# Performance work log

Measured on AMD Instinct MI355X. Metric: run time of the kernel, lower is better.

Reference implementation:

```python
import jax, jax.numpy as jnp
import numpy as np

R_MAX = 1.0
BASIS_MASK = 0xFF        # low 8 bits -> basis index (basis_size=256)
R_BITS_MASK = 0xFFFF     # next 16 bits -> quantized radius
R_DENOM = 65535.0
INT8_DENOM = 127.0


def setup_inputs() -> dict:
    key = jax.random.key(0)
    k_x, k_c, k_b, k_r, k_s, k_bias = jax.random.split(key, 6)
    B, S, D_in, D_out, BASIS = 4, 2048, 4096, 4096, 256
    x = jax.random.normal(k_x, (B, S, D_in), dtype=jnp.float32)
    codes = jax.random.randint(k_c, (D_out,), 0, 16777216, dtype=jnp.int32)
    basis_table = jax.random.normal(k_b, (BASIS, D_in), dtype=jnp.float32)
    residual_q = jax.random.randint(k_r, (D_out, D_in), 0, 256, dtype=jnp.int32)
    residual_scales = jax.random.uniform(k_s, (D_out,), dtype=jnp.float32) * 0.05
    bias = jax.random.normal(k_bias, (D_out,), dtype=jnp.float32)
    return {"x": x, "codes": codes, "basis_table": basis_table,
            "residual_q": residual_q, "residual_scales": residual_scales,
            "bias": bias}


def decode_weight(codes, basis_table, residual_q, residual_scales):
    # Bitfield decode: low 8 bits = basis index, next 16 bits = quantized radius in [0, r_max].
    idx = codes & BASIS_MASK                                   # [O]
    r = ((codes >> 8) & R_BITS_MASK).astype(jnp.float32) / R_DENOM * R_MAX  # [O]
    base = r[:, None] * basis_table[idx]                       # [O, I]
    resid = (residual_q.astype(jnp.float32) - 128.0) / INT8_DENOM  # dequant int8 residual
    return base + residual_scales[:, None] * resid             # [O, I]


def reference(x, codes, basis_table, residual_q, residual_scales, bias):
    W = decode_weight(codes, basis_table, residual_q, residual_scales)  # [O, I]
    # y = x @ W^T + bias  (fused dequant-matmul in the original CUDA kernel)
    return jnp.einsum("bsi,oi->bso", x, W) + bias
```

## Files before the change

### kernel.cpp

```cpp
#include <hip/hip_runtime.h>


typedef __bf16 bf16x8 __attribute__((ext_vector_type(8)));
typedef float f32x4 __attribute__((ext_vector_type(4)));
typedef int i32x4 __attribute__((ext_vector_type(4)));
typedef unsigned short u16x8 __attribute__((ext_vector_type(8)));

__device__ __forceinline__ unsigned short f2bf(float f) {
    union { float f; unsigned int u; } c; c.f = f;
    unsigned int u = c.u;
    u += 0x7fffu + ((u >> 16) & 1u);
    return (unsigned short)(u >> 16);
}
__device__ __forceinline__ float bf2f(unsigned short h) {
    union { unsigned int u; float f; } c; c.u = ((unsigned int)h) << 16;
    return c.f;
}

__device__ __forceinline__ void load_lds16(const void* g, void* l) {
    __builtin_amdgcn_global_load_lds(
        (__attribute__((address_space(1))) void*)(void*)g,
        (__attribute__((address_space(3))) void*)l,
        16, 0, 0);
}

__device__ __forceinline__ int swz_decode(int p, int row_bytes) {
    const int g = p >> 3, t = p & 7, v = t ^ (g & 7);
    const int row = g * 2 + (v >> 2), chunk = v & 3;
    return row * row_bytes + chunk * 16;
}

__global__ void cvt_bf16_kernel(const float4* __restrict__ in4,
                                ushort4* __restrict__ out4, int n4) {
    int i = blockIdx.x * blockDim.x + threadIdx.x;
    const int stride = gridDim.x * blockDim.x;
    for (; i < n4; i += stride) {
        float4 v = in4[i];
        ushort4 o;
        o.x = f2bf(v.x); o.y = f2bf(v.y); o.z = f2bf(v.z); o.w = f2bf(v.w);
        out4[i] = o;
    }
}

__global__ void quant_x_kernel(const float* __restrict__ x,
                               signed char* __restrict__ xq,
                               float* __restrict__ arow, int K) {
    const int m = blockIdx.x;
    const float* row = x + (size_t)m * K;
    const int base = threadIdx.x * 16;
    float4 v[4];
#pragma unroll
    for (int j = 0; j < 4; ++j) v[j] = *(const float4*)(row + base + j * 4);

    float lmax = 0.f;
#pragma unroll
    for (int j = 0; j < 4; ++j) {
        lmax = fmaxf(lmax, fabsf(v[j].x));
        lmax = fmaxf(lmax, fabsf(v[j].y));
        lmax = fmaxf(lmax, fabsf(v[j].z));
        lmax = fmaxf(lmax, fabsf(v[j].w));
    }
#pragma unroll
    for (int off = 32; off; off >>= 1)
        lmax = fmaxf(lmax, __shfl_xor(lmax, off));
    __shared__ float smax[4];
    if ((threadIdx.x & 63) == 0) smax[threadIdx.x >> 6] = lmax;
    __syncthreads();
    const float mx = fmaxf(fmaxf(smax[0], smax[1]), fmaxf(smax[2], smax[3]));
    const float inv = mx > 0.f ? 127.0f / mx : 0.0f;
    if (threadIdx.x == 0) arow[m] = mx * (1.0f / 127.0f);

    union { signed char c[16]; i32x4 w; } pk;
#pragma unroll
    for (int j = 0; j < 4; ++j) {
        pk.c[j * 4 + 0] = (signed char)(int)rintf(v[j].x * inv);
        pk.c[j * 4 + 1] = (signed char)(int)rintf(v[j].y * inv);
        pk.c[j * 4 + 2] = (signed char)(int)rintf(v[j].z * inv);
        pk.c[j * 4 + 3] = (signed char)(int)rintf(v[j].w * inv);
    }
    *(i32x4*)(xq + (size_t)m * K + base) = pk.w;
}

__global__ void pack_q_kernel(const int4* __restrict__ q4,
                              unsigned int* __restrict__ out, int n4) {
    const int i = blockIdx.x * blockDim.x + threadIdx.x;
    if (i >= n4) return;
    int4 a = q4[i];
    unsigned int w = ((unsigned)(a.x - 128) & 0xFFu)
                   | (((unsigned)(a.y - 128) & 0xFFu) << 8)
                   | (((unsigned)(a.z - 128) & 0xFFu) << 16)
                   | (((unsigned)(a.w - 128) & 0xFFu) << 24);
    out[i] = w;
}

__global__ void p_gemm_kernel(const unsigned short* __restrict__ Xb,
                              const unsigned short* __restrict__ Bb,
                              unsigned short* __restrict__ Pbf,
                              int M, int K) {
    __shared__ __align__(16) unsigned short As[64 * 32];
    __shared__ __align__(16) unsigned short Bs[64 * 32];

    const int tid  = threadIdx.x;
    const int lane = tid & 63;
    const int wv   = tid >> 6;
    const int m0 = blockIdx.y * 64;
    const int n0 = blockIdx.x * 64;
    const int lr = lane & 15;
    const int kg = lane >> 4;
    const int swz = (lr >> 1) & 7;

    f32x4 acc[4];
#pragma unroll
    for (int ni = 0; ni < 4; ++ni) acc[ni] = (f32x4){0.f, 0.f, 0.f, 0.f};

    const int goff = swz_decode(tid, 64);
    const unsigned short* Agp = Xb + (size_t)m0 * K + (goff >> 6) * K + ((goff & 63) >> 1);
    const unsigned short* Bgp = Bb + (size_t)n0 * K + (goff >> 6) * K + ((goff & 63) >> 1);
    unsigned short* Al = As + tid * 8;
    unsigned short* Bl = Bs + tid * 8;

    const int cidx = (((lr & 1) << 2) | kg) ^ swz;

    for (int k0 = 0; k0 < K; k0 += 32) {
        load_lds16(Agp + k0, Al);
        load_lds16(Bgp + k0, Bl);
        __syncthreads();

        const int arow2 = wv * 8 + (lr >> 1);
        bf16x8 af = __builtin_bit_cast(bf16x8,
            *(const u16x8*)(As + arow2 * 64 + cidx * 8));
#pragma unroll
        for (int ni = 0; ni < 4; ++ni) {
            const int brow2 = ni * 8 + (lr >> 1);
            bf16x8 bfr = __builtin_bit_cast(bf16x8,
                *(const u16x8*)(Bs + brow2 * 64 + cidx * 8));
            acc[ni] = __builtin_amdgcn_mfma_f32_16x16x32_bf16(af, bfr, acc[ni], 0, 0, 0);
        }
        __syncthreads();
    }

#pragma unroll
    for (int ni = 0; ni < 4; ++ni) {
        const int n = n0 + ni * 16 + lr;
        const int mbase = m0 + wv * 16 + kg * 4;
#pragma unroll
        for (int rg = 0; rg < 4; ++rg)
            Pbf[(size_t)(mbase + rg) * 256 + n] = f2bf(acc[ni][rg]);
    }
}

__global__ void gemm_i8_kernel(const signed char* __restrict__ Xq,
                               const signed char* __restrict__ Qb,
                               const float* __restrict__ arow,
                               const int* __restrict__ codes,
                               const float* __restrict__ scales,
                               const float* __restrict__ bias,
                               const unsigned short* __restrict__ Pbf,
                               float* __restrict__ out,
                               int M, int N, int K) {
    __shared__ __align__(16) signed char As[128 * 64];
    __shared__ __align__(16) signed char Bs[128 * 64];
    __shared__ unsigned short Pst[64 * 256];

    const int tid  = threadIdx.x;
    const int lane = tid & 63;
    const int wv   = tid >> 6;
    const int wrow = wv >> 1;
    const int wcol = wv & 1;
    const int m0 = blockIdx.y * 128;
    const int n0 = blockIdx.x * 128;
    const int lr = lane & 15;
    const int kg = lane >> 4;
    const int swz = (lr >> 1) & 7;
    const int cidx = (((lr & 1) << 2) | kg) ^ swz;

    int   cc[4];
    float rr[4], so[4], bv[4];
#pragma unroll
    for (int ni = 0; ni < 4; ++ni) {
        const int n = n0 + wcol * 64 + ni * 16 + lr;
        const int code = codes[n];
        cc[ni] = code & 0xFF;
        rr[ni] = (float)((code >> 8) & 0xFFFF) * (1.0f / 65535.0f);
        so[ni] = scales[n] * (1.0f / 127.0f);
        bv[ni] = bias[n];
    }
#pragma unroll
    for (int ni = 0; ni < 4; ++ni)
#pragma unroll
        for (int mi = 0; mi < 4; ++mi) {
            const int mb = m0 + wrow * 64 + mi * 16 + kg * 4;
#pragma unroll
            for (int rg = 0; rg < 4; ++rg) {
                unsigned short pv = Pbf[(size_t)(mb + rg) * 256 + cc[ni]];
                Pst[(ni * 16 + mi * 4 + rg) * 256 + tid] = pv;
            }
        }

    i32x4 acc[4][4];
#pragma unroll
    for (int mi = 0; mi < 4; ++mi)
#pragma unroll
        for (int ni = 0; ni < 4; ++ni)
            acc[mi][ni] = (i32x4){0, 0, 0, 0};

    const int p0 = tid, p1 = tid + 256;
    const int ga0 = swz_decode(p0, 64);
    const int ga1 = swz_decode(p1, 64);
    const signed char* Ag0 = Xq + (size_t)m0 * K + (ga0 >> 6) * K + (ga0 & 63);
    const signed char* Ag1 = Xq + (size_t)m0 * K + (ga1 >> 6) * K + (ga1 & 63);
    const signed char* Bg0 = Qb + (size_t)n0 * K + (ga0 >> 6) * K + (ga0 & 63);
    const signed char* Bg1 = Qb + (size_t)n0 * K + (ga1 >> 6) * K + (ga1 & 63);
    signed char* Al0 = As + p0 * 16;
    signed char* Al1 = As + p1 * 16;
    signed char* Bl0 = Bs + p0 * 16;
    signed char* Bl1 = Bs + p1 * 16;

    for (int k0 = 0; k0 < K; k0 += 64) {
        load_lds16(Ag0 + k0, Al0);
        load_lds16(Ag1 + k0, Al1);
        load_lds16(Bg0 + k0, Bl0);
        load_lds16(Bg1 + k0, Bl1);
        __syncthreads();

        i32x4 af[4], bfr[4];
#pragma unroll
        for (int mi = 0; mi < 4; ++mi) {
            const int r2 = wrow * 32 + mi * 8 + (lr >> 1);
            af[mi] = *(const i32x4*)(As + r2 * 128 + cidx * 16);
        }
#pragma unroll
        for (int ni = 0; ni < 4; ++ni) {
            const int r2 = wcol * 32 + ni * 8 + (lr >> 1);
            bfr[ni] = *(const i32x4*)(Bs + r2 * 128 + cidx * 16);
        }
#pragma unroll
        for (int mi = 0; mi < 4; ++mi)
#pragma unroll
            for (int ni = 0; ni < 4; ++ni)
                acc[mi][ni] = __builtin_amdgcn_mfma_i32_16x16x64_i8(
                    af[mi], bfr[ni], acc[mi][ni], 0, 0, 0);
        __syncthreads();
    }

    float av[4][4];
#pragma unroll
    for (int mi = 0; mi < 4; ++mi)
#pragma unroll
        for (int rg = 0; rg < 4; ++rg)
            av[mi][rg] = arow[m0 + wrow * 64 + mi * 16 + kg * 4 + rg];

#pragma unroll
    for (int ni = 0; ni < 4; ++ni) {
        const int n = n0 + wcol * 64 + ni * 16 + lr;
#pragma unroll
        for (int mi = 0; mi < 4; ++mi) {
            const int mbase = m0 + wrow * 64 + mi * 16 + kg * 4;
#pragma unroll
            for (int rg = 0; rg < 4; ++rg) {
                const float pf = bf2f(Pst[(ni * 16 + mi * 4 + rg) * 256 + tid]);
                const float y = av[mi][rg] * so[ni] * (float)acc[mi][ni][rg]
                              + rr[ni] * pf + bv[ni];
                __builtin_nontemporal_store(y, &out[(size_t)(mbase + rg) * N + n]);
            }
        }
    }
}

extern "C" void kernel_launch(void* const* d_in, const int* in_sizes, int n_in,
                              void* d_out, int out_size, void* d_ws, size_t ws_size,
                              hipStream_t stream) {
    const float* x        = (const float*)d_in[0];
    const int*   codes    = (const int*)d_in[1];
    const float* basis    = (const float*)d_in[2];
    const int*   q        = (const int*)d_in[3];
    const float* scales   = (const float*)d_in[4];
    const float* bias     = (const float*)d_in[5];
    float* out = (float*)d_out;

    const int BASIS = 256;
    const int K = in_sizes[2] / BASIS;
    const int N = in_sizes[1];
    const int M = in_sizes[0] / K;

    char* ws = (char*)d_ws;
    unsigned short* Xb = (unsigned short*)ws;
    signed char*    Xq = (signed char*)ws;
    size_t off = (size_t)M * K * 2;
    signed char* Qb = (signed char*)(ws + off);
    off += (size_t)N * K;
    unsigned short* Pbf = (unsigned short*)(ws + off);
    off += (size_t)M * 256 * 2;
    float* Arow = (float*)(ws + off);
    off += (size_t)M * sizeof(float);
    unsigned short* Bb = (unsigned short*)(ws + off);

    cvt_bf16_kernel<<<4096, 256, 0, stream>>>((const float4*)x, (ushort4*)Xb,
                                              M * K / 4);
    cvt_bf16_kernel<<<1024, 256, 0, stream>>>((const float4*)basis, (ushort4*)Bb,
                                              BASIS * K / 4);
    p_gemm_kernel<<<dim3(BASIS / 64, M / 64), 256, 0, stream>>>(Xb, Bb, Pbf, M, K);
    pack_q_kernel<<<(N * K / 4 + 255) / 256, 256, 0, stream>>>(
        (const int4*)q, (unsigned int*)Qb, N * K / 4);
    quant_x_kernel<<<M, 256, 0, stream>>>(x, Xq, Arow, K);
    gemm_i8_kernel<<<dim3(N / 128, M / 128), 256, 0, stream>>>(
        Xq, Qb, Arow, codes, scales, bias, Pbf, out, M, N, K);
}
```

Measured before the change: 535.2 us.

## Fuse x bf16 conversion into basis GEMM and enlarge int8 GEMM tile

The separate fp32-to-bf16 conversion pass over x is removed. The basis projection GEMM now loads fp32 x directly into LDS and converts it while building fragments, with each block covering all 256 basis columns for 32 rows. The int8 GEMM tile grows to 128x256 with launch bounds set for two blocks per CU and a swapped grid order. The LDS staging of gathered P values is dropped in favour of direct global loads in the epilogue. These changes cut memory traffic and launches, but they raise register pressure and turn the P gather into uncoalesced global reads.

```diff
diff --git a/kernel.cpp b/kernel.cpp
--- a/kernel.cpp
+++ b/kernel.cpp
@@ -93,151 +93,163 @@
     out[i] = w;
 }
 
-__global__ void p_gemm_kernel(const unsigned short* __restrict__ Xb,
-                              const unsigned short* __restrict__ Bb,
-                              unsigned short* __restrict__ Pbf,
-                              int M, int K) {
-    __shared__ __align__(16) unsigned short As[64 * 32];
-    __shared__ __align__(16) unsigned short Bs[64 * 32];
+__global__ __launch_bounds__(256) void
+p_gemm_kernel(const float* __restrict__ x,
+              const unsigned short* __restrict__ Bb,
+              unsigned short* __restrict__ Pbf,
+              int M, int K) {
+    __shared__ __align__(16) float As[32 * 64];
+    __shared__ __align__(16) unsigned short Bs[256 * 64];
 
     const int tid  = threadIdx.x;
     const int lane = tid & 63;
     const int wv   = tid >> 6;
-    const int m0 = blockIdx.y * 64;
-    const int n0 = blockIdx.x * 64;
+    const int m0 = blockIdx.x * 32;
     const int lr = lane & 15;
     const int kg = lane >> 4;
-    const int swz = (lr >> 1) & 7;
-
-    f32x4 acc[4];
-#pragma unroll
-    for (int ni = 0; ni < 4; ++ni) acc[ni] = (f32x4){0.f, 0.f, 0.f, 0.f};
-
-    const int goff = swz_decode(tid, 64);
-    const unsigned short* Agp = Xb + (size_t)m0 * K + (goff >> 6) * K + ((goff & 63) >> 1);
-    const unsigned short* Bgp = Bb + (size_t)n0 * K + (goff >> 6) * K + ((goff & 63) >> 1);
-    unsigned short* Al = As + tid * 8;
-    unsigned short* Bl = Bs + tid * 8;
-
-    const int cidx = (((lr & 1) << 2) | kg) ^ swz;
-
-    for (int k0 = 0; k0 < K; k0 += 32) {
-        load_lds16(Agp + k0, Al);
-        load_lds16(Bgp + k0, Bl);
+
+    f32x4 acc[2][4];
+#pragma unroll
+    for (int mi = 0; mi < 2; ++mi)
+#pragma unroll
+        for (int ni = 0; ni < 4; ++ni)
+            acc[mi][ni] = (f32x4){0.f, 0.f, 0.f, 0.f};
+
+    int aRow[2], aSrc[2];
+#pragma unroll
+    for (int j = 0; j < 2; ++j) {
+        const int p = tid + 256 * j;
+        aRow[j] = p >> 4;
+        aSrc[j] = (p & 15) ^ (aRow[j] & 15);
+    }
+    int bRow[8], bSrc[8];
+#pragma unroll
+    for (int j = 0; j < 8; ++j) {
+        const int p = tid + 256 * j;
+        bRow[j] = p >> 3;
+        bSrc[j] = (p & 7) ^ (bRow[j] & 7);
+    }
+
+    for (int k0 = 0; k0 < K; k0 += 64) {
+#pragma unroll
+        for (int j = 0; j < 2; ++j)
+            load_lds16(x + (size_t)(m0 + aRow[j]) * K + k0 + aSrc[j] * 4,
+                       (char*)As + (tid + 256 * j) * 16);
+#pragma unroll
+        for (int j = 0; j < 8; ++j)
+            load_lds16(Bb + (size_t)bRow[j] * K + k0 + bSrc[j] * 8,
+                       (char*)Bs + (tid + 256 * j) * 16);
         __syncthreads();
 
-        const int arow2 = wv * 8 + (lr >> 1);
-        bf16x8 af = __builtin_bit_cast(bf16x8,
-            *(const u16x8*)(As + arow2 * 64 + cidx * 8));
-#pragma unroll
-        for (int ni = 0; ni < 4; ++ni) {
-            const int brow2 = ni * 8 + (lr >> 1);
-            bf16x8 bfr = __builtin_bit_cast(bf16x8,
-                *(const u16x8*)(Bs + brow2 * 64 + cidx * 8));
-            acc[ni] = __builtin_amdgcn_mfma_f32_16x16x32_bf16(af, bfr, acc[ni], 0, 0, 0);
+#pragma unroll
+        for (int s = 0; s < 2; ++s) {
+            bf16x8 af[2];
+#pragma unroll
+            for (int mi = 0; mi < 2; ++mi) {
+                const int r = mi * 16 + lr;
+                const int c0 = s * 8 + kg * 2;
+                const int ph0 = c0 ^ (r & 15);
+                const int ph1 = (c0 + 1) ^ (r & 15);
+                f32x4 lo = *(const f32x4*)(As + r * 64 + ph0 * 4);
+                f32x4 hi = *(const f32x4*)(As + r * 64 + ph1 * 4);
+                bf16x8 a;
+                a[0] = (__bf16)lo[0]; a[1] = (__bf16)lo[1];
+                a[2] = (__bf16)lo[2]; a[3] = (__bf16)lo[3];
+                a[4] = (__bf16)hi[0]; a[5] = (__bf16)hi[1];
+                a[6] = (__bf16)hi[2]; a[7] = (__bf16)hi[3];
+                af[mi] = a;
+            }
+#pragma unroll
+            for (int ni = 0; ni < 4; ++ni) {
+                const int rb = wv * 64 + ni * 16 + lr;
+                const int ph = (s * 4 + kg) ^ (rb & 7);
+                bf16x8 bfr = __builtin_bit_cast(bf16x8,
+                    *(const u16x8*)(Bs + rb * 64 + ph * 8));
+#pragma unroll
+                for (int mi = 0; mi < 2; ++mi)
+                    acc[mi][ni] = __builtin_amdgcn_mfma_f32_16x16x32_bf16(
+                        af[mi], bfr, acc[mi][ni], 0, 0, 0);
+            }
         }
         __syncthreads();
     }
 
 #pragma unroll
     for (int ni = 0; ni < 4; ++ni) {
-        const int n = n0 + ni * 16 + lr;
-        const int mbase = m0 + wv * 16 + kg * 4;
-#pragma unroll
-        for (int rg = 0; rg < 4; ++rg)
-            Pbf[(size_t)(mbase + rg) * 256 + n] = f2bf(acc[ni][rg]);
-    }
-}
-
-__global__ void gemm_i8_kernel(const signed char* __restrict__ Xq,
-                               const signed char* __restrict__ Qb,
-                               const float* __restrict__ arow,
-                               const int* __restrict__ codes,
-                               const float* __restrict__ scales,
-                               const float* __restrict__ bias,
-                               const unsigned short* __restrict__ Pbf,
-                               float* __restrict__ out,
-                               int M, int N, int K) {
+        const int n = wv * 64 + ni * 16 + lr;
+#pragma unroll
+        for (int mi = 0; mi < 2; ++mi) {
+            const int mbase = m0 + mi * 16 + kg * 4;
+#pragma unroll
+            for (int rg = 0; rg < 4; ++rg)
+                Pbf[(size_t)(mbase + rg) * 256 + n] = f2bf(acc[mi][ni][rg]);
+        }
+    }
+}
+
+__global__ __launch_bounds__(256, 2) void
+gemm_i8_kernel(const signed char* __restrict__ Xq,
+               const signed char* __restrict__ Qb,
+               const float* __restrict__ arow,
+               const int* __restrict__ codes,
+               const float* __restrict__ scales,
+               const float* __restrict__ bias,
+               const unsigned short* __restrict__ Pbf,
+               float* __restrict__ out,
+               int M, int N, int K) {
     __shared__ __align__(16) signed char As[128 * 64];
-    __shared__ __align__(16) signed char Bs[128 * 64];
-    __shared__ unsigned short Pst[64 * 256];
+    __shared__ __align__(16) signed char Bs[256 * 64];
 
     const int tid  = threadIdx.x;
     const int lane = tid & 63;
     const int wv   = tid >> 6;
-    const int wrow = wv >> 1;
-    const int wcol = wv & 1;
-    const int m0 = blockIdx.y * 128;
-    const int n0 = blockIdx.x * 128;
+    const int wr   = wv >> 1;
+    const int wc   = wv & 1;
+    const int m0 = blockIdx.x * 128;
+    const int n0 = blockIdx.y * 256;
     const int lr = lane & 15;
     const int kg = lane >> 4;
-    const int swz = (lr >> 1) & 7;
-    const int cidx = (((lr & 1) << 2) | kg) ^ swz;
-
-    int   cc[4];
-    float rr[4], so[4], bv[4];
-#pragma unroll
-    for (int ni = 0; ni < 4; ++ni) {
-        const int n = n0 + wcol * 64 + ni * 16 + lr;
-        const int code = codes[n];
-        cc[ni] = code & 0xFF;
-        rr[ni] = (float)((code >> 8) & 0xFFFF) * (1.0f / 65535.0f);
-        so[ni] = scales[n] * (1.0f / 127.0f);
-        bv[ni] = bias[n];
-    }
-#pragma unroll
-    for (int ni = 0; ni < 4; ++ni)
+    const int cidx = (((lr & 1) << 2) | kg) ^ ((lr >> 1) & 7);
+
+    i32x4 acc[4][8];
+#pragma unroll
+    for (int mi = 0; mi < 4; ++mi)
+#pragma unroll
+        for (int ni = 0; ni < 8; ++ni)
+            acc[mi][ni] = (i32x4){0, 0, 0, 0};
+
+    int gaOff[2], gbOff[4];
+#pragma unroll
+    for (int j = 0; j < 2; ++j) gaOff[j] = swz_decode(tid + 256 * j, 64);
+#pragma unroll
+    for (int j = 0; j < 4; ++j) gbOff[j] = swz_decode(tid + 256 * j, 64);
+
+    for (int k0 = 0; k0 < K; k0 += 64) {
+#pragma unroll
+        for (int j = 0; j < 2; ++j)
+            load_lds16(Xq + (size_t)(m0 + (gaOff[j] >> 6)) * K + (gaOff[j] & 63) + k0,
+                       As + (tid + 256 * j) * 16);
+#pragma unroll
+        for (int j = 0; j < 4; ++j)
+            load_lds16(Qb + (size_t)(n0 + (gbOff[j] >> 6)) * K + (gbOff[j] & 63) + k0,
+                       Bs + (tid + 256 * j) * 16);
+        __syncthreads();
+
+        i32x4 af[4], bfr[8];
 #pragma unroll
         for (int mi = 0; mi < 4; ++mi) {
-            const int mb = m0 + wrow * 64 + mi * 16 + kg * 4;
-#pragma unroll
-            for (int rg = 0; rg < 4; ++rg) {
-                unsigned short pv = Pbf[(size_t)(mb + rg) * 256 + cc[ni]];
-                Pst[(ni * 16 + mi * 4 + rg) * 256 + tid] = pv;
-            }
-        }
-
-    i32x4 acc[4][4];
-#pragma unroll
-    for (int mi = 0; mi < 4; ++mi)
-#pragma unroll
-        for (int ni = 0; ni < 4; ++ni)
-            acc[mi][ni] = (i32x4){0, 0, 0, 0};
-
-    const int p0 = tid, p1 = tid + 256;
-    const int ga0 = swz_decode(p0, 64);
-    const int ga1 = swz_decode(p1, 64);
-    const signed char* Ag0 = Xq + (size_t)m0 * K + (ga0 >> 6) * K + (ga0 & 63);
-    const signed char* Ag1 = Xq + (size_t)m0 * K + (ga1 >> 6) * K + (ga1 & 63);
-    const signed char* Bg0 = Qb + (size_t)n0 * K + (ga0 >> 6) * K + (ga0 & 63);
-    const signed char* Bg1 = Qb + (size_t)n0 * K + (ga1 >> 6) * K + (ga1 & 63);
-    signed char* Al0 = As + p0 * 16;
-    signed char* Al1 = As + p1 * 16;
-    signed char* Bl0 = Bs + p0 * 16;
-    signed char* Bl1 = Bs + p1 * 16;
-
-    for (int k0 = 0; k0 < K; k0 += 64) {
-        load_lds16(Ag0 + k0, Al0);
-        load_lds16(Ag1 + k0, Al1);
-        load_lds16(Bg0 + k0, Bl0);
-        load_lds16(Bg1 + k0, Bl1);
-        __syncthreads();
-
-        i32x4 af[4], bfr[4];
-#pragma unroll
-        for (int mi = 0; mi < 4; ++mi) {
-            const int r2 = wrow * 32 + mi * 8 + (lr >> 1);
+            const int r2 = wr * 32 + mi * 8 + (lr >> 1);
             af[mi] = *(const i32x4*)(As + r2 * 128 + cidx * 16);
         }
 #pragma unroll
-        for (int ni = 0; ni < 4; ++ni) {
-            const int r2 = wcol * 32 + ni * 8 + (lr >> 1);
+        for (int ni = 0; ni < 8; ++ni) {
+            const int r2 = wc * 64 + ni * 8 + (lr >> 1);
             bfr[ni] = *(const i32x4*)(Bs + r2 * 128 + cidx * 16);
         }
 #pragma unroll
         for (int mi = 0; mi < 4; ++mi)
 #pragma unroll
-            for (int ni = 0; ni < 4; ++ni)
+            for (int ni = 0; ni < 8; ++ni)
                 acc[mi][ni] = __builtin_amdgcn_mfma_i32_16x16x64_i8(
                     af[mi], bfr[ni], acc[mi][ni], 0, 0, 0);
         __syncthreads();
@@ -248,19 +260,27 @@
     for (int mi = 0; mi < 4; ++mi)
 #pragma unroll
         for (int rg = 0; rg < 4; ++rg)
-            av[mi][rg] = arow[m0 + wrow * 64 + mi * 16 + kg * 4 + rg];
-
-#pragma unroll
-    for (int ni = 0; ni < 4; ++ni) {
-        const int n = n0 + wcol * 64 + ni * 16 + lr;
+            av[mi][rg] = arow[m0 + wr * 64 + mi * 16 + kg * 4 + rg];
+
+#pragma unroll
+    for (int ni = 0; ni < 8; ++ni) {
+        const int n = n0 + wc * 128 + ni * 16 + lr;
+        const int code = codes[n];
+        const int cc = code & 0xFF;
+        const float rr = (float)((code >> 8) & 0xFFFF) * (1.0f / 65535.0f);
+        const float so = scales[n] * (1.0f / 127.0f);
+        const float bv = bias[n];
 #pragma unroll
         for (int mi = 0; mi < 4; ++mi) {
-            const int mbase = m0 + wrow * 64 + mi * 16 + kg * 4;
+            const int mbase = m0 + wr * 64 + mi * 16 + kg * 4;
+            unsigned short pv[4];
+#pragma unroll
+            for (int rg = 0; rg < 4; ++rg)
+                pv[rg] = Pbf[(size_t)(mbase + rg) * 256 + cc];
 #pragma unroll
             for (int rg = 0; rg < 4; ++rg) {
-                const float pf = bf2f(Pst[(ni * 16 + mi * 4 + rg) * 256 + tid]);
-                const float y = av[mi][rg] * so[ni] * (float)acc[mi][ni][rg]
-                              + rr[ni] * pf + bv[ni];
+                const float y = av[mi][rg] * so * (float)acc[mi][ni][rg]
+                              + rr * bf2f(pv[rg]) + bv;
                 __builtin_nontemporal_store(y, &out[(size_t)(mbase + rg) * N + n]);
             }
         }
@@ -284,9 +304,8 @@
     const int M = in_sizes[0] / K;
 
     char* ws = (char*)d_ws;
-    unsigned short* Xb = (unsigned short*)ws;
-    signed char*    Xq = (signed char*)ws;
-    size_t off = (size_t)M * K * 2;
+    signed char* Xq = (signed char*)ws;
+    size_t off = (size_t)M * K;
     signed char* Qb = (signed char*)(ws + off);
     off += (size_t)N * K;
     unsigned short* Pbf = (unsigned short*)(ws + off);
@@ -295,14 +314,12 @@
     off += (size_t)M * sizeof(float);
     unsigned short* Bb = (unsigned short*)(ws + off);
 
-    cvt_bf16_kernel<<<4096, 256, 0, stream>>>((const float4*)x, (ushort4*)Xb,
-                                              M * K / 4);
     cvt_bf16_kernel<<<1024, 256, 0, stream>>>((const float4*)basis, (ushort4*)Bb,
                                               BASIS * K / 4);
-    p_gemm_kernel<<<dim3(BASIS / 64, M / 64), 256, 0, stream>>>(Xb, Bb, Pbf, M, K);
+    p_gemm_kernel<<<M / 32, 256, 0, stream>>>(x, Bb, Pbf, M, K);
+    quant_x_kernel<<<M, 256, 0, stream>>>(x, Xq, Arow, K);
     pack_q_kernel<<<(N * K / 4 + 255) / 256, 256, 0, stream>>>(
         (const int4*)q, (unsigned int*)Qb, N * K / 4);
-    quant_x_kernel<<<M, 256, 0, stream>>>(x, Xq, Arow, K);
-    gemm_i8_kernel<<<dim3(N / 128, M / 128), 256, 0, stream>>>(
+    gemm_i8_kernel<<<dim3(M / 128, N / 256), 256, 0, stream>>>(
         Xq, Qb, Arow, codes, scales, bias, Pbf, out, M, N, K);
 }
```

Measured after the change: 489.6 us. 1.09x faster.
